# Kernel tuning notes

Hardware: AMD Instinct MI355X
Metric: run time of the kernel (lower is better)

## Reference

```python
import jax, jax.numpy as jnp
import numpy as np


def _gcn_conv(x, src, dst, W, b, n_nodes):
    # PyG GCNConv: add self-loops, symmetric deg^{-1/2} normalization, then linear.
    xw = x @ W  # [N, H]
    # degree including self-loop (count of incoming edges at dst + 1)
    deg = jnp.zeros((n_nodes,), dtype=xw.dtype).at[dst].add(1.0) + 1.0
    dinv = jax.lax.rsqrt(deg)  # deg >= 1 always
    coef = (dinv[src] * dinv[dst])[:, None]  # [E, 1]
    out = jnp.zeros_like(xw).at[dst].add(xw[src] * coef)
    # self-loop edge i->i has norm dinv[i]^2
    out = out + xw * (dinv * dinv)[:, None]
    return out + b


def setup_inputs() -> dict:
    key = jax.random.key(0)
    ks = jax.random.split(key, 6)
    N, E, F, H, G = 200000, 600000, 128, 128, 64
    x = jax.random.normal(ks[0], (N, F), dtype=jnp.float32)
    edge_index = jax.random.randint(ks[1], (2, E), 0, N, dtype=jnp.int64)
    batch = jnp.sort(jax.random.randint(ks[2], (N,), 0, G, dtype=jnp.int64))
    W1 = jax.random.normal(ks[3], (F, H), dtype=jnp.float32) * (1.0 / np.sqrt(F))
    b1 = jnp.zeros((H,), dtype=jnp.float32)
    W2 = jax.random.normal(ks[4], (H, H), dtype=jnp.float32) * (1.0 / np.sqrt(H))
    b2 = jnp.zeros((H,), dtype=jnp.float32)
    return {"x": x, "edge_index": edge_index, "batch": batch, "num_graphs": G,
            "W1": W1, "b1": b1, "W2": W2, "b2": b2}


def reference(x, edge_index, batch, num_graphs, W1, b1, W2, b2):
    n_nodes = x.shape[0]
    # feature standardization (torch .std is unbiased, ddof=1)
    x = (x - x.mean(axis=0, keepdims=True)) / x.std(axis=0, keepdims=True, ddof=1)
    src, dst = edge_index[0], edge_index[1]
    h = jax.nn.relu(_gcn_conv(x, src, dst, W1, b1, n_nodes))
    # dropout p=0 -> identity
    h = jax.nn.relu(_gcn_conv(h, src, dst, W2, b2, n_nodes))
    # global_add_pool over batch ids
    return jax.ops.segment_sum(h, batch, num_segments=num_graphs)
```

## Files before the change

kernel.cpp:

```cpp
#include <hip/hip_runtime.h>

#define FDIM 128

typedef __attribute__((ext_vector_type(8))) short short8;
typedef __attribute__((ext_vector_type(4))) float f32x4;

__device__ inline unsigned short f2bf(float f) {
    unsigned int u = __float_as_uint(f);
    unsigned int r = u + 0x7FFFu + ((u >> 16) & 1u);
    return (unsigned short)(r >> 16);
}
__device__ inline float bf2f(unsigned short b) {
    return __uint_as_float((unsigned int)b << 16);
}
__device__ inline void bf8_fma(short8 v, float c, float* acc) {
#pragma unroll
    for (int k = 0; k < 8; ++k)
        acc[k] = fmaf(bf2f(((const unsigned short*)&v)[k]), c, acc[k]);
}

__global__ __launch_bounds__(256) void pre_combo(const float* __restrict__ x, int N,
                                                 float* __restrict__ partials, int statBlocks,
                                                 const int* __restrict__ dst, int E,
                                                 int* __restrict__ cnt) {
    if ((int)blockIdx.x >= statBlocks) {
        int e = (blockIdx.x - statBlocks) * 256 + threadIdx.x;
        if (e < E) atomicAdd(&cnt[dst[e]], 1);
        return;
    }
    const int c4 = threadIdx.x & 31;
    const int rg = threadIdx.x >> 5;
    float4 s = make_float4(0.f, 0.f, 0.f, 0.f);
    float4 q = make_float4(0.f, 0.f, 0.f, 0.f);
    for (long r = (long)blockIdx.x * 8 + rg; r < N; r += (long)statBlocks * 8) {
        float4 v = ((const float4*)x)[r * 32 + c4];
        s.x += v.x; s.y += v.y; s.z += v.z; s.w += v.w;
        q.x += v.x * v.x; q.y += v.y * v.y; q.z += v.z * v.z; q.w += v.w * v.w;
    }
    __shared__ float red[8][32][8];
    float* p = red[rg][c4];
    p[0] = s.x; p[1] = s.y; p[2] = s.z; p[3] = s.w;
    p[4] = q.x; p[5] = q.y; p[6] = q.z; p[7] = q.w;
    __syncthreads();
    if (rg == 0) {
#pragma unroll
        for (int g = 1; g < 8; ++g) {
            const float* o = red[g][c4];
#pragma unroll
            for (int j = 0; j < 8; ++j) red[0][c4][j] += o[j];
        }
        const float* r0 = red[0][c4];
        float* out = &partials[(size_t)blockIdx.x * 256];
        ((float4*)out)[c4] = make_float4(r0[0], r0[1], r0[2], r0[3]);
        ((float4*)(out + 128))[c4] = make_float4(r0[4], r0[5], r0[6], r0[7]);
    }
}

__global__ __launch_bounds__(256) void mid_combo(const int* __restrict__ cnt, int N,
                                                 int* __restrict__ start,
                                                 int* __restrict__ wcur,
                                                 int* __restrict__ counter,
                                                 float* __restrict__ dinv,
                                                 const float* __restrict__ partials,
                                                 int nblk, int offsBlocks,
                                                 const float* __restrict__ W1,
                                                 const float* __restrict__ W2,
                                                 unsigned short* __restrict__ WT1,
                                                 unsigned short* __restrict__ WT2,
                                                 float* __restrict__ bias0) {
    const int tid = threadIdx.x;
    if ((int)blockIdx.x < offsBlocks) {
        __shared__ int sh[256];
        __shared__ int base;
        int i = blockIdx.x * 256 + tid;
        int v = (i < N) ? cnt[i] : 0;
        sh[tid] = v;
        __syncthreads();
        for (int off = 1; off < 256; off <<= 1) {
            int t = (tid >= off) ? sh[tid - off] : 0;
            __syncthreads();
            sh[tid] += t;
            __syncthreads();
        }
        if (tid == 255) base = atomicAdd(counter, sh[255]);
        __syncthreads();
        int excl = base + sh[tid] - v;
        if (i < N) {
            start[i] = excl;
            wcur[i] = excl;
            dinv[i] = rsqrtf((float)v + 1.0f);
        }
        return;
    }
    const int b = blockIdx.x - offsBlocks;
    const int h = tid & 127;
    const int seg = tid >> 7;
    if (b < 8) {
        __shared__ float red[32][32];
        __shared__ float scol[32], mean_sh[16], rstd_sh[16];
        const int rg = tid >> 3;
        const int f = tid & 7;
        const int colbase = (f < 4) ? (b * 16 + f * 4) : (128 + b * 16 + (f - 4) * 4);
        float4 a = make_float4(0.f, 0.f, 0.f, 0.f);
        for (int row = rg; row < nblk; row += 32) {
            float4 v = *(const float4*)&partials[(size_t)row * 256 + colbase];
            a.x += v.x; a.y += v.y; a.z += v.z; a.w += v.w;
        }
        *(float4*)&red[rg][f * 4] = a;
        __syncthreads();
        if (tid < 32) {
            float s = 0.f;
#pragma unroll
            for (int r = 0; r < 32; ++r) s += red[r][tid];
            scol[tid] = s;
        }
        __syncthreads();
        if (tid < 16) {
            float m = scol[tid] / (float)N;
            float var = (scol[16 + tid] - (float)N * m * m) / (float)(N - 1);
            mean_sh[tid] = m;
            rstd_sh[tid] = rsqrtf(var);
        }
        __syncthreads();
        float acc = 0.f;
#pragma unroll
        for (int jj = 0; jj < 8; ++jj) {
            int jl = seg * 8 + jj;
            int j2 = b * 16 + jl;
            float w = W1[j2 * FDIM + h] * rstd_sh[jl];
            WT1[h * FDIM + j2] = f2bf(w);
            acc += mean_sh[jl] * w;
        }
        unsafeAtomicAdd(&bias0[h], -acc);
    } else {
#pragma unroll
        for (int jj = 0; jj < 8; ++jj) {
            int j2 = (b - 8) * 16 + seg * 8 + jj;
            WT2[h * FDIM + j2] = f2bf(W2[j2 * FDIM + h]);
        }
    }
}

__global__ __launch_bounds__(256) void gemm1_fill(const float* __restrict__ A,
                                                  const unsigned short* __restrict__ WT,
                                                  const float* __restrict__ bias,
                                                  unsigned short* __restrict__ C, int M,
                                                  int gemmBlocks,
                                                  const int* __restrict__ src,
                                                  const int* __restrict__ dst,
                                                  const float* __restrict__ dinv,
                                                  int* __restrict__ wcur,
                                                  int2* __restrict__ edata, int E) {
    const int tid = threadIdx.x;
    if ((int)blockIdx.x >= gemmBlocks) {
        int e = (blockIdx.x - gemmBlocks) * 256 + tid;
        if (e < E) {
            int s = src[e], d = dst[e];
            int pos = atomicAdd(&wcur[d], 1);
            edata[pos] = make_int2(s, __float_as_int(dinv[s] * dinv[d]));
        }
        return;
    }
    constexpr int LDA = 136;
    __shared__ unsigned short Alds[64 * LDA];
    __shared__ unsigned short Wlds[FDIM * LDA];
    const int row0 = blockIdx.x * 64;

    for (int i = tid; i < FDIM * 16; i += 256) {
        int r = i >> 4, g = i & 15;
        *(int4*)&Wlds[r * LDA + g * 8] = *(const int4*)&WT[r * FDIM + g * 8];
    }
    for (int i = tid; i < 64 * 32; i += 256) {
        int r = i >> 5, c4 = i & 31;
        int row = row0 + r;
        float4 v = make_float4(0.f, 0.f, 0.f, 0.f);
        if (row < M) v = ((const float4*)A)[(size_t)row * 32 + c4];
        ushort4 p;
        p.x = f2bf(v.x); p.y = f2bf(v.y); p.z = f2bf(v.z); p.w = f2bf(v.w);
        *(ushort4*)&Alds[r * LDA + c4 * 4] = p;
    }
    __syncthreads();

    const int lane = tid & 63;
    const int wave = tid >> 6;
    const int m16 = lane & 15;
    const int quad = lane >> 4;

    f32x4 acc[8];
#pragma unroll
    for (int t = 0; t < 8; ++t) acc[t] = (f32x4){0.f, 0.f, 0.f, 0.f};

    const unsigned short* Abase = &Alds[(wave * 16 + m16) * LDA + quad * 8];
    const unsigned short* Wbase = &Wlds[m16 * LDA + quad * 8];
#pragma unroll
    for (int s = 0; s < 4; ++s) {
        short8 a = *(const short8*)&Abase[s * 32];
#pragma unroll
        for (int t = 0; t < 8; ++t) {
            short8 b = *(const short8*)&Wbase[t * 16 * LDA + s * 32];
            acc[t] = __builtin_amdgcn_mfma_f32_16x16x32_bf16(b, a, acc[t], 0, 0, 0);
        }
    }

    const int r = row0 + wave * 16 + m16;
    if (r < M) {
#pragma unroll
        for (int t = 0; t < 8; ++t) {
            ushort4 o;
            o.x = f2bf(acc[t][0] + bias[t * 16 + quad * 4 + 0]);
            o.y = f2bf(acc[t][1] + bias[t * 16 + quad * 4 + 1]);
            o.z = f2bf(acc[t][2] + bias[t * 16 + quad * 4 + 2]);
            o.w = f2bf(acc[t][3] + bias[t * 16 + quad * 4 + 3]);
            *(ushort4*)&C[(size_t)r * FDIM + t * 16 + quad * 4] = o;
        }
    }
}

__global__ __launch_bounds__(256) void gemm_mfma2(const unsigned short* __restrict__ A,
                                                  const unsigned short* __restrict__ WT,
                                                  unsigned short* __restrict__ C, int M) {
    constexpr int LDA = 136;
    __shared__ unsigned short Alds[64 * LDA];
    __shared__ unsigned short Wlds[FDIM * LDA];
    const int tid = threadIdx.x;
    const int row0 = blockIdx.x * 64;

    for (int i = tid; i < FDIM * 16; i += 256) {
        int r = i >> 4, g = i & 15;
        *(int4*)&Wlds[r * LDA + g * 8] = *(const int4*)&WT[r * FDIM + g * 8];
    }
    for (int i = tid; i < 64 * 16; i += 256) {
        int r = i >> 4, g = i & 15;
        int row = row0 + r;
        int4 v = make_int4(0, 0, 0, 0);
        if (row < M) v = *(const int4*)&A[(size_t)row * FDIM + g * 8];
        *(int4*)&Alds[r * LDA + g * 8] = v;
    }
    __syncthreads();

    const int lane = tid & 63;
    const int wave = tid >> 6;
    const int m16 = lane & 15;
    const int quad = lane >> 4;

    f32x4 acc[8];
#pragma unroll
    for (int t = 0; t < 8; ++t) acc[t] = (f32x4){0.f, 0.f, 0.f, 0.f};

    const unsigned short* Abase = &Alds[(wave * 16 + m16) * LDA + quad * 8];
    const unsigned short* Wbase = &Wlds[m16 * LDA + quad * 8];
#pragma unroll
    for (int s = 0; s < 4; ++s) {
        short8 a = *(const short8*)&Abase[s * 32];
#pragma unroll
        for (int t = 0; t < 8; ++t) {
            short8 b = *(const short8*)&Wbase[t * 16 * LDA + s * 32];
            acc[t] = __builtin_amdgcn_mfma_f32_16x16x32_bf16(b, a, acc[t], 0, 0, 0);
        }
    }

    const int r = row0 + wave * 16 + m16;
    if (r < M) {
#pragma unroll
        for (int t = 0; t < 8; ++t) {
            ushort4 o;
            o.x = f2bf(acc[t][0]); o.y = f2bf(acc[t][1]);
            o.z = f2bf(acc[t][2]); o.w = f2bf(acc[t][3]);
            *(ushort4*)&C[(size_t)r * FDIM + t * 16 + quad * 4] = o;
        }
    }
}

template <bool POOL>
__global__ __launch_bounds__(256) void aggregate(const unsigned short* __restrict__ xw,
                                                 const float* __restrict__ dinv,
                                                 const int* __restrict__ start,
                                                 const int* __restrict__ cnt,
                                                 const int2* __restrict__ edata,
                                                 const float* __restrict__ bvec,
                                                 unsigned short* __restrict__ out,
                                                 const int* __restrict__ batch,
                                                 float* __restrict__ pool_part,
                                                 int* __restrict__ ptag,
                                                 float* __restrict__ pooled, int N) {
    const int base = blockIdx.x * 16;
    const int node = base + (threadIdx.x >> 4);
    const int l8 = threadIdx.x & 15;
    const bool active = node < N;
    if (!POOL && !active) return;
    const int nidx = active ? node : (N - 1);

    float dv = dinv[nidx];
    float d2 = dv * dv;
    float4 b0 = ((const float4*)bvec)[l8 * 2];
    float4 b1 = ((const float4*)bvec)[l8 * 2 + 1];
    float acc[8] = {b0.x, b0.y, b0.z, b0.w, b1.x, b1.y, b1.z, b1.w};
    short8 sv = *(const short8*)&xw[(size_t)nidx * FDIM + l8 * 8];
    bf8_fma(sv, d2, acc);

    int j = start[nidx];
    const int s1 = j + (active ? cnt[nidx] : 0);
    for (; j + 4 <= s1; j += 4) {
        int2 e0 = edata[j], e1 = edata[j + 1], e2 = edata[j + 2], e3 = edata[j + 3];
        short8 u0 = *(const short8*)&xw[(size_t)e0.x * FDIM + l8 * 8];
        short8 u1 = *(const short8*)&xw[(size_t)e1.x * FDIM + l8 * 8];
        short8 u2 = *(const short8*)&xw[(size_t)e2.x * FDIM + l8 * 8];
        short8 u3 = *(const short8*)&xw[(size_t)e3.x * FDIM + l8 * 8];
        bf8_fma(u0, __int_as_float(e0.y), acc);
        bf8_fma(u1, __int_as_float(e1.y), acc);
        bf8_fma(u2, __int_as_float(e2.y), acc);
        bf8_fma(u3, __int_as_float(e3.y), acc);
    }
    for (; j < s1; ++j) {
        int2 ed = edata[j];
        short8 u = *(const short8*)&xw[(size_t)ed.x * FDIM + l8 * 8];
        bf8_fma(u, __int_as_float(ed.y), acc);
    }

    if constexpr (!POOL) {
        short8 o;
#pragma unroll
        for (int k = 0; k < 8; ++k)
            ((unsigned short*)&o)[k] = f2bf(fmaxf(acc[k], 0.f));
        *(short8*)&out[(size_t)node * FDIM + l8 * 8] = o;
    } else {
        float r[8];
#pragma unroll
        for (int k = 0; k < 8; ++k) r[k] = active ? fmaxf(acc[k], 0.f) : 0.f;
        int g0 = batch[base];
        int g1 = batch[min(base + 15, N - 1)];
        if (g0 == g1) {
            __shared__ float red[16][FDIM];
            float* dst = &red[threadIdx.x >> 4][l8 * 8];
            *(float4*)dst = make_float4(r[0], r[1], r[2], r[3]);
            *(float4*)(dst + 4) = make_float4(r[4], r[5], r[6], r[7]);
            __syncthreads();
            if (threadIdx.x < FDIM) {
                float s = 0.f;
#pragma unroll
                for (int i = 0; i < 16; ++i) s += red[i][threadIdx.x];
                pool_part[(size_t)blockIdx.x * FDIM + threadIdx.x] = s;
                if (threadIdx.x == 0) ptag[blockIdx.x] = g0;
            }
        } else {
            if (threadIdx.x == 0) ptag[blockIdx.x] = -1;
            if (active) {
                int g = batch[node];
#pragma unroll
                for (int k = 0; k < 8; ++k)
                    unsafeAtomicAdd(&pooled[g * FDIM + l8 * 8 + k], r[k]);
            }
        }
    }
}

__global__ __launch_bounds__(128) void pool_reduce(const float* __restrict__ pool_part,
                                                   const int* __restrict__ ptag,
                                                   int nslots, float* __restrict__ out) {
    int per = (nslots + gridDim.x - 1) / gridDim.x;
    int s0 = blockIdx.x * per;
    int s1 = min(s0 + per, nslots);
    int t = threadIdx.x;
    float acc = 0.f;
    int cur = -1;
    for (int s = s0; s < s1; ++s) {
        int g = ptag[s];
        if (g < 0) continue;
        if (g != cur) {
            if (cur >= 0) unsafeAtomicAdd(&out[cur * FDIM + t], acc);
            acc = 0.f;
            cur = g;
        }
        acc += pool_part[(size_t)s * FDIM + t];
    }
    if (cur >= 0) unsafeAtomicAdd(&out[cur * FDIM + t], acc);
}

extern "C" void kernel_launch(void* const* d_in, const int* in_sizes, int n_in,
                              void* d_out, int out_size, void* d_ws, size_t ws_size,
                              hipStream_t stream) {
    const float* x = (const float*)d_in[0];
    const int* ei = (const int*)d_in[1];
    const int* batch = (const int*)d_in[2];
    const float* W1 = (const float*)d_in[4];
    const float* b1 = (const float*)d_in[5];
    const float* W2 = (const float*)d_in[6];
    const float* b2 = (const float*)d_in[7];

    const int N = in_sizes[2];
    const int E = in_sizes[1] / 2;
    const int* srcp = ei;
    const int* dstp = ei + E;

    const size_t NF = (size_t)N * FDIM;
    const int aggGrid = (N + 15) / 16;
    unsigned short* bufA = (unsigned short*)d_ws;
    unsigned short* bufB = bufA + NF;
    int* cnt = (int*)(bufB + NF);
    int* counter = cnt + N;
    float* bias0 = (float*)(counter + 4);
    float* dinv = bias0 + FDIM;
    int* start = (int*)(dinv + N);
    int* wcur = start + N;
    unsigned short* WT1 = (unsigned short*)(wcur + N);
    unsigned short* WT2 = WT1 + FDIM * FDIM;
    int2* edata = (int2*)(WT2 + FDIM * FDIM);
    float* pool_part = (float*)(edata + E);
    int* ptag = (int*)(pool_part + (size_t)aggGrid * FDIM);
    float* partials = (float*)edata;
    const int STAT_BLOCKS = 512;

    hipMemsetAsync(cnt, 0, ((size_t)N + 4 + FDIM) * sizeof(int), stream);
    hipMemsetAsync(d_out, 0, (size_t)out_size * sizeof(float), stream);

    const int degBlocks = (E + 255) / 256;
    const int offsBlocks = (N + 255) / 256;
    const int gemmGrid = (N + 63) / 64;

    pre_combo<<<STAT_BLOCKS + degBlocks, 256, 0, stream>>>(x, N, partials, STAT_BLOCKS,
                                                           dstp, E, cnt);
    mid_combo<<<offsBlocks + 16, 256, 0, stream>>>(cnt, N, start, wcur, counter, dinv,
                                                   partials, STAT_BLOCKS, offsBlocks,
                                                   W1, W2, WT1, WT2, bias0);

    gemm1_fill<<<gemmGrid + degBlocks, 256, 0, stream>>>(x, WT1, bias0, bufA, N, gemmGrid,
                                                         srcp, dstp, dinv, wcur, edata, E);
    aggregate<false><<<aggGrid, 256, 0, stream>>>(bufA, dinv, start, cnt, edata, b1,
                                                  bufB, nullptr, nullptr, nullptr,
                                                  nullptr, N);

    gemm_mfma2<<<gemmGrid, 256, 0, stream>>>(bufB, WT2, bufA, N);
    aggregate<true><<<aggGrid, 256, 0, stream>>>(bufA, dinv, start, cnt, edata, b2,
                                                 nullptr, batch, pool_part, ptag,
                                                 (float*)d_out, N);
    pool_reduce<<<256, 128, 0, stream>>>(pool_part, ptag, aggGrid, (float*)d_out);
}
```

Measured before the change: 404.2 us.

## Fuse layer-1 aggregation with layer-2 GEMM and read weights from global

Merges the first-layer neighbor aggregation (with bias and ReLU) and the second-layer GEMM into one kernel. Each 16-node block stages its aggregated rows in LDS and multiplies them by WT2 with MFMA, so the intermediate h never makes a round trip through HBM and one launch is removed. Both GEMMs now read weight fragments directly from global/L2 instead of staging the full weight matrix in LDS. This cuts LDS use and raises occupancy (gemm1 gets a launch-bounds occupancy hint), at the cost of repeated global weight loads and small 16-row MFMA tiles.

Result: slower. 433.6 us (+7.3%).

```diff
diff --git a/kernel.cpp b/kernel.cpp
--- a/kernel.cpp
+++ b/kernel.cpp
@@ -141,16 +141,16 @@
     }
 }
 
-__global__ __launch_bounds__(256) void gemm1_fill(const float* __restrict__ A,
-                                                  const unsigned short* __restrict__ WT,
-                                                  const float* __restrict__ bias,
-                                                  unsigned short* __restrict__ C, int M,
-                                                  int gemmBlocks,
-                                                  const int* __restrict__ src,
-                                                  const int* __restrict__ dst,
-                                                  const float* __restrict__ dinv,
-                                                  int* __restrict__ wcur,
-                                                  int2* __restrict__ edata, int E) {
+__global__ __launch_bounds__(256, 4) void gemm1_fill(const float* __restrict__ A,
+                                                     const unsigned short* __restrict__ WT,
+                                                     const float* __restrict__ bias,
+                                                     unsigned short* __restrict__ C, int M,
+                                                     int gemmBlocks,
+                                                     const int* __restrict__ src,
+                                                     const int* __restrict__ dst,
+                                                     const float* __restrict__ dinv,
+                                                     int* __restrict__ wcur,
+                                                     int2* __restrict__ edata, int E) {
     const int tid = threadIdx.x;
     if ((int)blockIdx.x >= gemmBlocks) {
         int e = (blockIdx.x - gemmBlocks) * 256 + tid;
@@ -163,13 +163,8 @@
     }
     constexpr int LDA = 136;
     __shared__ unsigned short Alds[64 * LDA];
-    __shared__ unsigned short Wlds[FDIM * LDA];
     const int row0 = blockIdx.x * 64;
 
-    for (int i = tid; i < FDIM * 16; i += 256) {
-        int r = i >> 4, g = i & 15;
-        *(int4*)&Wlds[r * LDA + g * 8] = *(const int4*)&WT[r * FDIM + g * 8];
-    }
     for (int i = tid; i < 64 * 32; i += 256) {
         int r = i >> 5, c4 = i & 31;
         int row = row0 + r;
@@ -191,13 +186,13 @@
     for (int t = 0; t < 8; ++t) acc[t] = (f32x4){0.f, 0.f, 0.f, 0.f};
 
     const unsigned short* Abase = &Alds[(wave * 16 + m16) * LDA + quad * 8];
-    const unsigned short* Wbase = &Wlds[m16 * LDA + quad * 8];
+    const unsigned short* Wg = &WT[(size_t)m16 * FDIM + quad * 8];
 #pragma unroll
     for (int s = 0; s < 4; ++s) {
         short8 a = *(const short8*)&Abase[s * 32];
 #pragma unroll
         for (int t = 0; t < 8; ++t) {
-            short8 b = *(const short8*)&Wbase[t * 16 * LDA + s * 32];
+            short8 b = *(const short8*)&Wg[t * 16 * FDIM + s * 32];
             acc[t] = __builtin_amdgcn_mfma_f32_16x16x32_bf16(b, a, acc[t], 0, 0, 0);
         }
     }
@@ -216,58 +211,90 @@
     }
 }
 
-__global__ __launch_bounds__(256) void gemm_mfma2(const unsigned short* __restrict__ A,
-                                                  const unsigned short* __restrict__ WT,
-                                                  unsigned short* __restrict__ C, int M) {
-    constexpr int LDA = 136;
-    __shared__ unsigned short Alds[64 * LDA];
-    __shared__ unsigned short Wlds[FDIM * LDA];
-    const int tid = threadIdx.x;
-    const int row0 = blockIdx.x * 64;
-
-    for (int i = tid; i < FDIM * 16; i += 256) {
-        int r = i >> 4, g = i & 15;
-        *(int4*)&Wlds[r * LDA + g * 8] = *(const int4*)&WT[r * FDIM + g * 8];
-    }
-    for (int i = tid; i < 64 * 16; i += 256) {
-        int r = i >> 4, g = i & 15;
-        int row = row0 + r;
-        int4 v = make_int4(0, 0, 0, 0);
-        if (row < M) v = *(const int4*)&A[(size_t)row * FDIM + g * 8];
-        *(int4*)&Alds[r * LDA + g * 8] = v;
+__global__ __launch_bounds__(256) void agg_gemm2(const unsigned short* __restrict__ xw,
+                                                 const float* __restrict__ dinv,
+                                                 const int* __restrict__ start,
+                                                 const int* __restrict__ cnt,
+                                                 const int2* __restrict__ edata,
+                                                 const float* __restrict__ bvec,
+                                                 const unsigned short* __restrict__ WT2,
+                                                 unsigned short* __restrict__ out,
+                                                 int N) {
+    const int base = blockIdx.x * 16;
+    const int node = base + (threadIdx.x >> 4);
+    const int l8 = threadIdx.x & 15;
+    const bool active = node < N;
+    const int nidx = active ? node : (N - 1);
+
+    float dv = dinv[nidx];
+    float d2 = dv * dv;
+    float4 b0 = ((const float4*)bvec)[l8 * 2];
+    float4 b1v = ((const float4*)bvec)[l8 * 2 + 1];
+    float acc[8] = {b0.x, b0.y, b0.z, b0.w, b1v.x, b1v.y, b1v.z, b1v.w};
+    short8 sv = *(const short8*)&xw[(size_t)nidx * FDIM + l8 * 8];
+    bf8_fma(sv, d2, acc);
+
+    int j = start[nidx];
+    const int s1 = j + (active ? cnt[nidx] : 0);
+    for (; j + 4 <= s1; j += 4) {
+        int2 e0 = edata[j], e1 = edata[j + 1], e2 = edata[j + 2], e3 = edata[j + 3];
+        short8 u0 = *(const short8*)&xw[(size_t)e0.x * FDIM + l8 * 8];
+        short8 u1 = *(const short8*)&xw[(size_t)e1.x * FDIM + l8 * 8];
+        short8 u2 = *(const short8*)&xw[(size_t)e2.x * FDIM + l8 * 8];
+        short8 u3 = *(const short8*)&xw[(size_t)e3.x * FDIM + l8 * 8];
+        bf8_fma(u0, __int_as_float(e0.y), acc);
+        bf8_fma(u1, __int_as_float(e1.y), acc);
+        bf8_fma(u2, __int_as_float(e2.y), acc);
+        bf8_fma(u3, __int_as_float(e3.y), acc);
+    }
+    for (; j < s1; ++j) {
+        int2 ed = edata[j];
+        short8 u = *(const short8*)&xw[(size_t)ed.x * FDIM + l8 * 8];
+        bf8_fma(u, __int_as_float(ed.y), acc);
+    }
+
+    constexpr int LDH = 136;
+    __shared__ unsigned short hlds[16 * LDH];
+    {
+        ushort4 o0, o1;
+        if (active) {
+            o0.x = f2bf(fmaxf(acc[0], 0.f)); o0.y = f2bf(fmaxf(acc[1], 0.f));
+            o0.z = f2bf(fmaxf(acc[2], 0.f)); o0.w = f2bf(fmaxf(acc[3], 0.f));
+            o1.x = f2bf(fmaxf(acc[4], 0.f)); o1.y = f2bf(fmaxf(acc[5], 0.f));
+            o1.z = f2bf(fmaxf(acc[6], 0.f)); o1.w = f2bf(fmaxf(acc[7], 0.f));
+        } else {
+            o0.x = 0; o0.y = 0; o0.z = 0; o0.w = 0;
+            o1.x = 0; o1.y = 0; o1.z = 0; o1.w = 0;
+        }
+        unsigned short* hp = &hlds[(threadIdx.x >> 4) * LDH + l8 * 8];
+        *(ushort4*)hp = o0;
+        *(ushort4*)(hp + 4) = o1;
     }
     __syncthreads();
 
-    const int lane = tid & 63;
-    const int wave = tid >> 6;
+    const int lane = threadIdx.x & 63;
+    const int wave = threadIdx.x >> 6;
     const int m16 = lane & 15;
     const int quad = lane >> 4;
-
-    f32x4 acc[8];
-#pragma unroll
-    for (int t = 0; t < 8; ++t) acc[t] = (f32x4){0.f, 0.f, 0.f, 0.f};
-
-    const unsigned short* Abase = &Alds[(wave * 16 + m16) * LDA + quad * 8];
-    const unsigned short* Wbase = &Wlds[m16 * LDA + quad * 8];
+    f32x4 c0 = (f32x4){0.f, 0.f, 0.f, 0.f};
+    f32x4 c1 = (f32x4){0.f, 0.f, 0.f, 0.f};
+    const unsigned short* Abase = &hlds[m16 * LDH + quad * 8];
+    const unsigned short* Wg = &WT2[(size_t)(wave * 32 + m16) * FDIM + quad * 8];
 #pragma unroll
     for (int s = 0; s < 4; ++s) {
         short8 a = *(const short8*)&Abase[s * 32];
-#pragma unroll
-        for (int t = 0; t < 8; ++t) {
-            short8 b = *(const short8*)&Wbase[t * 16 * LDA + s * 32];
-            acc[t] = __builtin_amdgcn_mfma_f32_16x16x32_bf16(b, a, acc[t], 0, 0, 0);
-        }
-    }
-
-    const int r = row0 + wave * 16 + m16;
-    if (r < M) {
-#pragma unroll
-        for (int t = 0; t < 8; ++t) {
-            ushort4 o;
-            o.x = f2bf(acc[t][0]); o.y = f2bf(acc[t][1]);
-            o.z = f2bf(acc[t][2]); o.w = f2bf(acc[t][3]);
-            *(ushort4*)&C[(size_t)r * FDIM + t * 16 + quad * 4] = o;
-        }
+        short8 w0 = *(const short8*)&Wg[s * 32];
+        short8 w1 = *(const short8*)&Wg[16 * FDIM + s * 32];
+        c0 = __builtin_amdgcn_mfma_f32_16x16x32_bf16(w0, a, c0, 0, 0, 0);
+        c1 = __builtin_amdgcn_mfma_f32_16x16x32_bf16(w1, a, c1, 0, 0, 0);
+    }
+    const int r = base + m16;
+    if (r < N) {
+        ushort4 o;
+        o.x = f2bf(c0[0]); o.y = f2bf(c0[1]); o.z = f2bf(c0[2]); o.w = f2bf(c0[3]);
+        *(ushort4*)&out[(size_t)r * FDIM + wave * 32 + quad * 4] = o;
+        o.x = f2bf(c1[0]); o.y = f2bf(c1[1]); o.z = f2bf(c1[2]); o.w = f2bf(c1[3]);
+        *(ushort4*)&out[(size_t)r * FDIM + wave * 32 + 16 + quad * 4] = o;
     }
 }
 
@@ -425,12 +452,11 @@
 
     gemm1_fill<<<gemmGrid + degBlocks, 256, 0, stream>>>(x, WT1, bias0, bufA, N, gemmGrid,
                                                          srcp, dstp, dinv, wcur, edata, E);
-    aggregate<false><<<aggGrid, 256, 0, stream>>>(bufA, dinv, start, cnt, edata, b1,
-                                                  bufB, nullptr, nullptr, nullptr,
-                                                  nullptr, N);
-
-    gemm_mfma2<<<gemmGrid, 256, 0, stream>>>(bufB, WT2, bufA, N);
-    aggregate<true><<<aggGrid, 256, 0, stream>>>(bufA, dinv, start, cnt, edata, b2,
+
+    agg_gemm2<<<aggGrid, 256, 0, stream>>>(bufA, dinv, start, cnt, edata, b1, WT2,
+                                           bufB, N);
+
+    aggregate<true><<<aggGrid, 256, 0, stream>>>(bufB, dinv, start, cnt, edata, b2,
                                                  nullptr, batch, pool_part, ptag,
                                                  (float*)d_out, N);
     pool_reduce<<<256, 128, 0, stream>>>(pool_part, ptag, aggGrid, (float*)d_out);
```
